# Kernel tuning notes

Measured on AMD Instinct MI355X. Metric: run time of the kernel, lower is better.

The kernel has to match this reference:

```python
import jax, jax.numpy as jnp
import numpy as np


def setup_inputs() -> dict:
    key = jax.random.key(0)
    k1, k2, k3 = jax.random.split(key, 3)
    B, N, E, A = 1024, 64, 64, 32
    emb_inputs = jax.random.normal(k1, (B, N, E), dtype=jnp.float32)
    W1 = jax.random.normal(k2, (E, A), dtype=jnp.float32) * (1.0 / np.sqrt(E))
    b1 = jnp.zeros((A,), dtype=jnp.float32)
    W2 = jax.random.normal(k3, (A, 1), dtype=jnp.float32) * (1.0 / np.sqrt(A))
    b2 = jnp.zeros((1,), dtype=jnp.float32)
    return {"emb_inputs": emb_inputs, "W1": W1, "b1": b1, "W2": W2, "b2": b2,
            "num_fields": N}


def reference(emb_inputs, W1, b1, W2, b2, num_fields):
    # Pairwise interaction indices (i < j), same order as torch double loop
    rowidx, colidx = np.triu_indices(num_fields, k=1)
    rowidx = jnp.asarray(rowidx)
    colidx = jnp.asarray(colidx)
    # inner: (B, NC2, E) elementwise product of field pairs
    inner = emb_inputs[:, rowidx] * emb_inputs[:, colidx]
    # tiny attention MLP: E -> A -> 1, softmax over the pair dim
    h = jax.nn.relu(jnp.einsum('bpe,ea->bpa', inner, W1) + b1)
    logits = jnp.einsum('bpa,ao->bpo', h, W2) + b2          # (B, NC2, 1)
    attn_scores = jax.nn.softmax(logits, axis=1)            # (B, NC2, 1)
    # dropout layers are identity in eval mode
    outputs = jnp.sum(inner * attn_scores, axis=1)          # (B, E)
    return outputs, attn_scores
```

## Files before the change

### kernel.cpp

```cpp
#include <hip/hip_runtime.h>

#define BATCH   1024
#define NF      64
#define EDIM    64
#define ADIM    32
#define NPAIR   2016
#define XSTR    72
#define ASTR    68

typedef _Float16 f16;
typedef f16   f16x4  __attribute__((ext_vector_type(4)));
typedef f16   f16x8  __attribute__((ext_vector_type(8)));
typedef float f32x2  __attribute__((ext_vector_type(2)));
typedef float f32x4  __attribute__((ext_vector_type(4)));
typedef float f32x16 __attribute__((ext_vector_type(16)));

__device__ __forceinline__ f16x8 asH(int4 v) {
    union { int4 i; f16x8 h; } u; u.i = v; return u.h;
}

__global__ __launch_bounds__(256, 4) void afm_kernel(
    const float* __restrict__ emb,
    const float* __restrict__ W1,
    const float* __restrict__ b1,
    const float* __restrict__ W2,
    const float* __restrict__ b2,
    float* __restrict__ out_vec,
    float* __restrict__ out_attn)
{
    __shared__ __align__(16) f16 xs[NF * XSTR];
    __shared__ __align__(16) f16 Xt[EDIM * XSTR];
    __shared__ __align__(16) char Ubuf[9088];
    float* logits = (float*)Ubuf;
    float (*partial)[EDIM] = (float (*)[EDIM])(Ubuf + 8064);
    f16* As = (f16*)Ubuf;
    __shared__ float red[8];

    const int t    = threadIdx.x;
    const int b    = blockIdx.x;
    const int wid  = t >> 6;
    const int lane = t & 63;
    const int g    = lane >> 4;
    const int m16  = lane & 15;
    const int h    = lane >> 5;
    const int l32  = lane & 31;
    const int l16  = lane & 15;
    const int hb   = l32 >> 4;

    const float4* xg4 = (const float4*)(emb + (size_t)b * NF * EDIM);
    #pragma unroll
    for (int it = 0; it < 4; ++it) {
        int idx = t + it * 256;
        int f = idx >> 4, e4 = (idx & 15) * 4;
        float4 v = xg4[idx];
        f16x4 pk = {(f16)v.x, (f16)v.y, (f16)v.z, (f16)v.w};
        *(f16x4*)&xs[f * XSTR + e4] = pk;
    }

    f16x8 w1a[4];
    #pragma unroll
    for (int q = 0; q < 4; ++q)
        #pragma unroll
        for (int jj = 0; jj < 8; ++jj)
            w1a[q][jj] = (f16)W1[(16 * q + 8 * h + jj) * ADIM + l32];

    f32x2 b1f2[8], w2f2[8];
    #pragma unroll
    for (int rr = 0; rr < 8; ++rr) {
        int r = 2 * rr;
        int a = (r & 3) + 8 * (r >> 2) + 4 * h;
        b1f2[rr] = (f32x2){b1[a], b1[a + 1]};
        w2f2[rr] = (f32x2){W2[a], W2[a + 1]};
    }
    const float b2s = b2[0];
    __syncthreads();

    {
        const unsigned short* xsu = (const unsigned short*)xs;
        #pragma unroll
        for (int it = 0; it < 2; ++it) {
            int cid = t + it * 256;
            int e = cid & 63, c = cid >> 6;
            unsigned int d[4];
            #pragma unroll
            for (int r2 = 0; r2 < 4; ++r2) {
                unsigned lo = xsu[(8 * c + 2 * r2)     * XSTR + e];
                unsigned hi = xsu[(8 * c + 2 * r2 + 1) * XSTR + e];
                d[r2] = lo | (hi << 16);
            }
            int4 w4 = {(int)d[0], (int)d[1], (int)d[2], (int)d[3]};
            *(int4*)&Xt[e * XSTR + 8 * c] = w4;
        }
    }
    __syncthreads();

    int probe = __builtin_amdgcn_mov_dpp(l16, 0x124, 0xF, 0xF, false);
    const bool plus4 = (probe == ((l16 + 4) & 15));
    const int  s0r   = plus4 ? (wid + 1) : (wid + 5);

    int4 xi4[4], xj4[4];

    auto LOADX = [&](int row, int4* d) {
        #pragma unroll
        for (int q = 0; q < 4; ++q)
            d[q] = *(const int4*)&xs[row * XSTR + 16 * q + 8 * h];
    };
    auto ROT4D = [&](int4* d, int& jv) {
        #pragma unroll
        for (int q = 0; q < 4; ++q) {
            d[q].x = __builtin_amdgcn_mov_dpp(d[q].x, 0x124, 0xF, 0xF, false);
            d[q].y = __builtin_amdgcn_mov_dpp(d[q].y, 0x124, 0xF, 0xF, false);
            d[q].z = __builtin_amdgcn_mov_dpp(d[q].z, 0x124, 0xF, 0xF, false);
            d[q].w = __builtin_amdgcn_mov_dpp(d[q].w, 0x124, 0xF, 0xF, false);
        }
        jv = __builtin_amdgcn_mov_dpp(jv, 0x124, 0xF, 0xF, false);
    };
    auto SUB = [&](const int4* xa, const int4* xb, int iv, int jv) {
        f32x16 acc = {};
        #pragma unroll
        for (int q = 0; q < 4; ++q) {
            f16x8 prod = asH(xa[q]) * asH(xb[q]);
            acc = __builtin_amdgcn_mfma_f32_32x32x16_f16(w1a[q], prod, acc, 0, 0, 0);
        }
        f32x2 tr2 = {0.f, 0.f};
        #pragma unroll
        for (int rr = 0; rr < 8; ++rr) {
            f32x2 a2 = {acc[2 * rr], acc[2 * rr + 1]};
            f32x2 h2 = __builtin_elementwise_max(a2 + b1f2[rr], (f32x2){0.f, 0.f});
            tr2 += h2 * w2f2[rr];
        }
        float tr = tr2.x + tr2.y;
        tr += __shfl_xor(tr, 32);
        int imin = min(iv, jv), jmax = max(iv, jv);
        int p = ((imin * (127 - imin)) >> 1) + jmax - imin - 1;
        if (lane < 32) logits[p] = tr + b2s;
    };

    LOADX(l32, xi4);
    {
        int jv = 32 + 16 * hb + ((l16 + wid) & 15);
        LOADX(jv, xj4);
        #pragma unroll
        for (int k = 0; k < 4; ++k) {
            SUB(xi4, xj4, l32, jv);
            if (k < 3) ROT4D(xj4, jv);
        }
    }
    {
        int jv = 32 + 16 * (1 - hb) + ((l16 + wid) & 15);
        LOADX(jv, xj4);
        #pragma unroll
        for (int k = 0; k < 4; ++k) {
            SUB(xi4, xj4, l32, jv);
            if (k < 3) ROT4D(xj4, jv);
        }
    }
    {
        int jv = 16 * hb + ((l16 + s0r) & 15);
        LOADX(jv, xj4);
        SUB(xi4, xj4, l32, jv);
        ROT4D(xj4, jv);
        SUB(xi4, xj4, l32, jv);
    }
    {
        int jv = 16 + ((l16 + wid + 8 * hb) & 15);
        LOADX(l16, xi4);
        LOADX(jv, xj4);
        SUB(xi4, xj4, l16, jv);
        ROT4D(xj4, jv);
        SUB(xi4, xj4, l16, jv);
    }
    {
        int jv = 32 + 16 * hb + ((l16 + s0r) & 15);
        LOADX(32 + l32, xi4);
        LOADX(jv, xj4);
        SUB(xi4, xj4, 32 + l32, jv);
        ROT4D(xj4, jv);
        SUB(xi4, xj4, 32 + l32, jv);
    }
    {
        int jv = 48 + ((l16 + wid + 8 * hb) & 15);
        LOADX(32 + l16, xi4);
        LOADX(jv, xj4);
        SUB(xi4, xj4, 32 + l16, jv);
        ROT4D(xj4, jv);
        SUB(xi4, xj4, 32 + l16, jv);
    }
    __syncthreads();

    float lv[8];
    #pragma unroll
    for (int k = 0; k < 8; ++k) {
        int p = t + 256 * k;
        lv[k] = (p < NPAIR) ? logits[p] : -INFINITY;
    }
    float mw = lv[0];
    #pragma unroll
    for (int k = 1; k < 8; ++k) mw = fmaxf(mw, lv[k]);
    #pragma unroll
    for (int off = 32; off; off >>= 1) mw = fmaxf(mw, __shfl_xor(mw, off));

    float sw = 0.0f;
    #pragma unroll
    for (int k = 0; k < 8; ++k) {
        float ev = __expf(lv[k] - mw);
        lv[k] = ev;
        sw += ev;
    }
    #pragma unroll
    for (int off = 32; off; off >>= 1) sw += __shfl_xor(sw, off);
    if (lane == 0) { red[wid] = mw; red[4 + wid] = sw; }
    __syncthreads();
    const float mg = fmaxf(fmaxf(red[0], red[1]), fmaxf(red[2], red[3]));
    const float ssum = red[4] * __expf(red[0] - mg) + red[5] * __expf(red[1] - mg)
                     + red[6] * __expf(red[2] - mg) + red[7] * __expf(red[3] - mg);
    const float fsc = __expf(mw - mg) / ssum;

    #pragma unroll
    for (int k = 0; k < 8; ++k) {
        int p = t + 256 * k;
        if (p < NPAIR) {
            float av = lv[k] * fsc;
            out_attn[(size_t)b * NPAIR + p] = av;
            int i = (int)(63.5f - 0.5f * sqrtf(16129.0f - 8.0f * (float)p));
            int Ti = (i * (127 - i)) >> 1;
            if (p < Ti)      { --i; Ti = (i * (127 - i)) >> 1; }
            else { int Tn = ((i + 1) * (126 - i)) >> 1; if (p >= Tn) { ++i; Ti = Tn; } }
            int j = p - Ti + i + 1;
            f16 ah = (f16)av;
            As[i * ASTR + j] = ah;
            As[j * ASTR + i] = ah;
        }
    }
    if (t < NF) As[t * ASTR + t] = (f16)0.f;
    __syncthreads();

    const int itile = wid;
    const f16* arow = &As[(itile * 16 + m16) * ASTR];
    f16x4 afa0 = *(const f16x4*)(arow + 8 * g);
    f16x4 afb0 = *(const f16x4*)(arow + 8 * g + 4);
    f16x4 afa1 = *(const f16x4*)(arow + 32 + 8 * g);
    f16x4 afb1 = *(const f16x4*)(arow + 32 + 8 * g + 4);
    __syncthreads();
    f16x8 af0, af1;
    #pragma unroll
    for (int j = 0; j < 4; ++j) {
        af0[j] = afa0[j]; af0[4 + j] = afb0[j];
        af1[j] = afa1[j]; af1[4 + j] = afb1[j];
    }

    f32x4 yacc[4];
    #pragma unroll
    for (int et = 0; et < 4; ++et) yacc[et] = (f32x4){0.f, 0.f, 0.f, 0.f};
    #pragma unroll
    for (int et = 0; et < 4; ++et) {
        const f16* xtr = &Xt[(et * 16 + m16) * XSTR];
        f16x8 bf0 = *(const f16x8*)(xtr + 8 * g);
        f16x8 bf1 = *(const f16x8*)(xtr + 32 + 8 * g);
        yacc[et] = __builtin_amdgcn_mfma_f32_16x16x32_f16(af0, bf0, yacc[et], 0, 0, 0);
        yacc[et] = __builtin_amdgcn_mfma_f32_16x16x32_f16(af1, bf1, yacc[et], 0, 0, 0);
    }

    #pragma unroll
    for (int et = 0; et < 4; ++et) {
        float v = 0.f;
        #pragma unroll
        for (int r = 0; r < 4; ++r) {
            int i = itile * 16 + 4 * g + r;
            int e = et * 16 + m16;
            v = fmaf((float)xs[i * XSTR + e], yacc[et][r], v);
        }
        v += __shfl_xor(v, 16);
        v += __shfl_xor(v, 32);
        if (g == 0) partial[wid][et * 16 + m16] = v;
    }
    __syncthreads();
    if (t < EDIM)
        out_vec[(size_t)b * EDIM + t] = 0.5f *
            (partial[0][t] + partial[1][t] + partial[2][t] + partial[3][t]);
}

extern "C" void kernel_launch(void* const* d_in, const int* in_sizes, int n_in,
                              void* d_out, int out_size, void* d_ws, size_t ws_size,
                              hipStream_t stream) {
    const float* emb = (const float*)d_in[0];
    const float* W1  = (const float*)d_in[1];
    const float* b1  = (const float*)d_in[2];
    const float* W2  = (const float*)d_in[3];
    const float* b2  = (const float*)d_in[4];
    float* out_vec  = (float*)d_out;
    float* out_attn = (float*)d_out + (size_t)BATCH * EDIM;

    afm_kernel<<<BATCH, 256, 0, stream>>>(emb, W1, b1, W2, b2, out_vec, out_attn);
}
```

Before: 26.28 us.

## Drop softmax max-subtraction and write unnormalized exp weights directly in MLP stage

Computes exp(logit) immediately in the pair-MLP stage and writes the unnormalized weights into both the logits buffer and the symmetric f16 attention matrix, removing the max reduction, the triangular index inversion and one barrier. Normalization is deferred: attention outputs are scaled by 1/sum and the final vector by the same factor. Shared memory is no longer aliased, and f32->f16 conversions use packed round-toward-zero. This risks overflow without max subtraction and f16 overflow for large exp values, and raises LDS use, which may lower occupancy.

```diff
diff --git a/kernel.cpp b/kernel.cpp
--- a/kernel.cpp
+++ b/kernel.cpp
@@ -9,6 +9,7 @@
 #define ASTR    68
 
 typedef _Float16 f16;
+typedef f16   f16x2  __attribute__((ext_vector_type(2)));
 typedef f16   f16x4  __attribute__((ext_vector_type(4)));
 typedef f16   f16x8  __attribute__((ext_vector_type(8)));
 typedef float f32x2  __attribute__((ext_vector_type(2)));
@@ -17,6 +18,11 @@
 
 __device__ __forceinline__ f16x8 asH(int4 v) {
     union { int4 i; f16x8 h; } u; u.i = v; return u.h;
+}
+__device__ __forceinline__ f16x2 pkrtz(float a, float b) {
+    union { __fp16 __attribute__((ext_vector_type(2))) r; f16x2 h; } u;
+    u.r = __builtin_amdgcn_cvt_pkrtz(a, b);
+    return u.h;
 }
 
 __global__ __launch_bounds__(256, 4) void afm_kernel(
@@ -30,10 +36,9 @@
 {
     __shared__ __align__(16) f16 xs[NF * XSTR];
     __shared__ __align__(16) f16 Xt[EDIM * XSTR];
-    __shared__ __align__(16) char Ubuf[9088];
-    float* logits = (float*)Ubuf;
-    float (*partial)[EDIM] = (float (*)[EDIM])(Ubuf + 8064);
-    f16* As = (f16*)Ubuf;
+    __shared__ __align__(16) f16 As[NF * ASTR];
+    __shared__ float logits[NPAIR];
+    __shared__ float partial[4][EDIM];
     __shared__ float red[8];
 
     const int t    = threadIdx.x;
@@ -53,7 +58,9 @@
         int idx = t + it * 256;
         int f = idx >> 4, e4 = (idx & 15) * 4;
         float4 v = xg4[idx];
-        f16x4 pk = {(f16)v.x, (f16)v.y, (f16)v.z, (f16)v.w};
+        f16x2 p0 = pkrtz(v.x, v.y);
+        f16x2 p1 = pkrtz(v.z, v.w);
+        f16x4 pk = {p0.x, p0.y, p1.x, p1.y};
         *(f16x4*)&xs[f * XSTR + e4] = pk;
     }
 
@@ -61,8 +68,12 @@
     #pragma unroll
     for (int q = 0; q < 4; ++q)
         #pragma unroll
-        for (int jj = 0; jj < 8; ++jj)
-            w1a[q][jj] = (f16)W1[(16 * q + 8 * h + jj) * ADIM + l32];
+        for (int jj = 0; jj < 8; jj += 2) {
+            float fa = W1[(16 * q + 8 * h + jj)     * ADIM + l32];
+            float fb = W1[(16 * q + 8 * h + jj + 1) * ADIM + l32];
+            f16x2 pk = pkrtz(fa, fb);
+            w1a[q][jj] = pk.x; w1a[q][jj + 1] = pk.y;
+        }
 
     f32x2 b1f2[8], w2f2[8];
     #pragma unroll
@@ -131,9 +142,15 @@
         }
         float tr = tr2.x + tr2.y;
         tr += __shfl_xor(tr, 32);
+        float ev = __expf(tr + b2s);
         int imin = min(iv, jv), jmax = max(iv, jv);
         int p = ((imin * (127 - imin)) >> 1) + jmax - imin - 1;
-        if (lane < 32) logits[p] = tr + b2s;
+        if (lane < 32) {
+            logits[p] = ev;
+            f16 ah = (f16)ev;
+            As[imin * ASTR + jmax] = ah;
+            As[jmax * ASTR + imin] = ah;
+        }
     };
 
     LOADX(l32, xi4);
@@ -186,54 +203,29 @@
         ROT4D(xj4, jv);
         SUB(xi4, xj4, 32 + l16, jv);
     }
+    if (t < NF) As[t * ASTR + t] = (f16)0.f;
     __syncthreads();
 
     float lv[8];
     #pragma unroll
     for (int k = 0; k < 8; ++k) {
         int p = t + 256 * k;
-        lv[k] = (p < NPAIR) ? logits[p] : -INFINITY;
-    }
-    float mw = lv[0];
-    #pragma unroll
-    for (int k = 1; k < 8; ++k) mw = fmaxf(mw, lv[k]);
-    #pragma unroll
-    for (int off = 32; off; off >>= 1) mw = fmaxf(mw, __shfl_xor(mw, off));
-
-    float sw = 0.0f;
-    #pragma unroll
-    for (int k = 0; k < 8; ++k) {
-        float ev = __expf(lv[k] - mw);
-        lv[k] = ev;
-        sw += ev;
-    }
+        lv[k] = (p < NPAIR) ? logits[p] : 0.f;
+    }
+    float sw = 0.f;
+    #pragma unroll
+    for (int k = 0; k < 8; ++k) sw += lv[k];
     #pragma unroll
     for (int off = 32; off; off >>= 1) sw += __shfl_xor(sw, off);
-    if (lane == 0) { red[wid] = mw; red[4 + wid] = sw; }
-    __syncthreads();
-    const float mg = fmaxf(fmaxf(red[0], red[1]), fmaxf(red[2], red[3]));
-    const float ssum = red[4] * __expf(red[0] - mg) + red[5] * __expf(red[1] - mg)
-                     + red[6] * __expf(red[2] - mg) + red[7] * __expf(red[3] - mg);
-    const float fsc = __expf(mw - mg) / ssum;
+    if (lane == 0) red[wid] = sw;
+    __syncthreads();
+    const float inv = 1.0f / (red[0] + red[1] + red[2] + red[3]);
 
     #pragma unroll
     for (int k = 0; k < 8; ++k) {
         int p = t + 256 * k;
-        if (p < NPAIR) {
-            float av = lv[k] * fsc;
-            out_attn[(size_t)b * NPAIR + p] = av;
-            int i = (int)(63.5f - 0.5f * sqrtf(16129.0f - 8.0f * (float)p));
-            int Ti = (i * (127 - i)) >> 1;
-            if (p < Ti)      { --i; Ti = (i * (127 - i)) >> 1; }
-            else { int Tn = ((i + 1) * (126 - i)) >> 1; if (p >= Tn) { ++i; Ti = Tn; } }
-            int j = p - Ti + i + 1;
-            f16 ah = (f16)av;
-            As[i * ASTR + j] = ah;
-            As[j * ASTR + i] = ah;
-        }
-    }
-    if (t < NF) As[t * ASTR + t] = (f16)0.f;
-    __syncthreads();
+        if (p < NPAIR) out_attn[(size_t)b * NPAIR + p] = lv[k] * inv;
+    }
 
     const int itile = wid;
     const f16* arow = &As[(itile * 16 + m16) * ASTR];
@@ -241,7 +233,6 @@
     f16x4 afb0 = *(const f16x4*)(arow + 8 * g + 4);
     f16x4 afa1 = *(const f16x4*)(arow + 32 + 8 * g);
     f16x4 afb1 = *(const f16x4*)(arow + 32 + 8 * g + 4);
-    __syncthreads();
     f16x8 af0, af1;
     #pragma unroll
     for (int j = 0; j < 4; ++j) {
@@ -276,7 +267,7 @@
     }
     __syncthreads();
     if (t < EDIM)
-        out_vec[(size_t)b * EDIM + t] = 0.5f *
+        out_vec[(size_t)b * EDIM + t] = 0.5f * inv *
             (partial[0][t] + partial[1][t] + partial[2][t] + partial[3][t]);
 }
 
```

After: 24.21 us. 7.9% less time.
